# Kernel tuning notes

Measured on AMD Instinct MI355X. Metric: run time of the kernel, lower is better.

## Reference

```python
import jax, jax.numpy as jnp
import numpy as np

B, S, DIM = 2, 2048, 2048
H = 16
Q_LORA, KV_LORA = 1536, 512
D_NOPE, D_ROPE, D_V = 128, 64, 128
D_QK = D_NOPE + D_ROPE  # 192
SCALE = D_QK ** -0.5
EPS = 1e-6
NEG = -1e30


def rmsnorm(x, w):
    return x * jax.lax.rsqrt(jnp.mean(x * x, axis=-1, keepdims=True) + EPS) * w


def apply_rope(x, cos, sin):
    # x: [..., S, ..., d] with adjacent-pair complex layout (torch view_as_complex)
    d2 = x.shape[-1] // 2
    xr = x.reshape(x.shape[:-1] + (d2, 2))
    x0, x1 = xr[..., 0], xr[..., 1]
    bshape = (1, cos.shape[0]) + (1,) * (x.ndim - 3) + (d2,)
    c, s = cos.reshape(bshape), sin.reshape(bshape)
    o0 = x0 * c - x1 * s
    o1 = x0 * s + x1 * c
    return jnp.stack([o0, o1], axis=-1).reshape(x.shape)


def setup_inputs() -> dict:
    key = jax.random.key(0)
    ks = jax.random.split(key, 6)
    inv_freq = 1.0 / (10000.0 ** (np.arange(0, D_ROPE, 2, dtype=np.float32) / D_ROPE))
    ang = np.arange(S, dtype=np.float32)[:, None] * inv_freq[None, :]  # [S, 32]
    return {
        "x": jax.random.normal(ks[0], (B, S, DIM), jnp.float32),
        "wq_a": jax.random.normal(ks[1], (Q_LORA, DIM), jnp.float32) * (DIM ** -0.5),
        "q_norm_w": jnp.ones((Q_LORA,), jnp.float32),
        "wq_b": jax.random.normal(ks[2], (H * D_QK, Q_LORA), jnp.float32) * (Q_LORA ** -0.5),
        "wkv_a": jax.random.normal(ks[3], (KV_LORA + D_ROPE, DIM), jnp.float32) * (DIM ** -0.5),
        "kv_norm_w": jnp.ones((KV_LORA,), jnp.float32),
        "wkv_b": jax.random.normal(ks[4], (H * (D_NOPE + D_V), KV_LORA), jnp.float32) * (KV_LORA ** -0.5),
        "wo": jax.random.normal(ks[5], (DIM, H * D_V), jnp.float32) * ((H * D_V) ** -0.5),
        "cos": jnp.asarray(np.cos(ang)),
        "sin": jnp.asarray(np.sin(ang)),
    }


def reference(x, wq_a, q_norm_w, wq_b, wkv_a, kv_norm_w, wkv_b, wo, cos, sin):
    b, s, _ = x.shape
    # low-rank query projection: wq_b(q_norm(wq_a(x)))
    q = jnp.einsum('bsd,rd->bsr', x, wq_a)
    q = rmsnorm(q, q_norm_w)
    q = jnp.einsum('bsr,or->bso', q, wq_b).reshape(b, s, H, D_QK)
    q_nope, q_pe = q[..., :D_NOPE], q[..., D_NOPE:]
    q_pe = apply_rope(q_pe, cos, sin)  # [b,s,h,64]

    # joint kv latent + rope key
    kv = jnp.einsum('bsd,od->bso', x, wkv_a)
    kv_c, k_pe = kv[..., :KV_LORA], kv[..., KV_LORA:]
    k_pe = apply_rope(k_pe, cos, sin)          # [b,t,64]
    kv_c = rmsnorm(kv_c, kv_norm_w)            # [b,t,c] latent kv cache

    # absorbed wkv_b: [H, d_nope+d_v, c]
    wkv_b_r = wkv_b.reshape(H, D_NOPE + D_V, KV_LORA)
    w_nope, w_v = wkv_b_r[:, :D_NOPE, :], wkv_b_r[:, D_NOPE:, :]

    q_abs = jnp.einsum('bshd,hdc->bshc', q_nope, w_nope)  # absorb K up-proj into q
    scores = (jnp.einsum('bshc,btc->bsht', q_abs, kv_c) +
              jnp.einsum('bshr,btr->bsht', q_pe, k_pe)) * SCALE

    causal = jnp.tril(jnp.ones((s, s), bool))  # [s, t]
    scores = jnp.where(causal[:, None, :], scores, NEG)

    attn = jax.nn.softmax(scores.astype(jnp.float32), axis=-1).astype(x.dtype)
    o = jnp.einsum('bsht,btc->bshc', attn, kv_c)       # attend in latent space
    o = jnp.einsum('bshc,hdc->bshd', o, w_v)           # absorb V up-proj
    out = jnp.einsum('bsf,of->bso', o.reshape(b, s, H * D_V), wo)
    return out
```

## Files before the change

### kernel.cpp

```cpp
#include <hip/hip_runtime.h>
#include <hip/hip_bf16.h>
#include <stdint.h>

#define B_    2
#define S_    2048
#define DIM_  2048
#define H_    16
#define QL_   1536
#define KVL_  512
#define DN_   128
#define DR_   64
#define DV_   128
#define DQK_  192
#define NKV_  576
#define NKVP_ 640
#define BS_   (B_*S_)
#define SCALE_ 0.07216878364870322f

typedef __hip_bfloat16 bf16;
typedef float f32x4 __attribute__((ext_vector_type(4)));
typedef short bf16x8 __attribute__((ext_vector_type(8)));

#define BMT 128
#define BNT 128
#define BKT 64

__device__ __forceinline__ void gload_lds16(const void* g, void* l) {
#if __has_builtin(__builtin_amdgcn_global_load_lds)
  __builtin_amdgcn_global_load_lds(
      (const __attribute__((address_space(1))) void*)g,
      (__attribute__((address_space(3))) void*)l, 16, 0, 0);
#else
  *(uint4*)l = *(const uint4*)g;
#endif
}

template <int K, int LDA, int LDB, int LDC, int FLAGS>
__global__ __launch_bounds__(512, 4) void gemm_t(
    const bf16* __restrict__ A, long saz,
    const bf16* __restrict__ Bm, long sbz,
    void* __restrict__ Cv, long scz,
    void* __restrict__ Cv2)
{
  int z = blockIdx.z;
  A  += (long)z * saz;
  Bm += (long)z * sbz;
  long coff = (long)z * scz;

  int gx = gridDim.x;
  int lin = blockIdx.y * gx + blockIdx.x;
  int nwg = gx * gridDim.y;
  int wg = (lin & 7) * (nwg >> 3) + (lin >> 3);
  int ry = wg / gx, col0 = (wg % gx) * BNT;

  int tid = threadIdx.x, lane = tid & 63, wave = tid >> 6;
  int wm = (wave >> 2) * 64, wn = (wave & 3) * 32;
  int quad = lane >> 4, l16 = lane & 15;

  __shared__ __align__(16) bf16 Asm[BMT * BKT];
  __shared__ __align__(16) bf16 Bsm[BNT * BKT];

  const int npass = (FLAGS & 16) ? 2 : 1;
  const int nty = gridDim.y * ((FLAGS & 16) ? 2 : 1);

  for (int p = 0; p < npass; ++p) {
    int rt = (p == 0) ? ry : (nty - 1 - ry);
    int row0 = rt * BMT;

    if (FLAGS & 2) { if (col0 > row0 + (BMT - 1)) continue; }
    int kend = K;
    if (FLAGS & 4) { int lim = row0 + BMT; if (lim < kend) kend = lim; }

    f32x4 acc[4][2] = {};

    for (int k0 = 0; k0 < kend; k0 += BKT) {
      __syncthreads();
#pragma unroll
      for (int t = 0; t < 2; ++t) {
        int c = (wave * 2 + t) * 64 + lane;
        int m = c >> 3, jx = c & 7, j = jx ^ (m & 7);
        gload_lds16(A  + (long)((row0 + m) * LDA + k0 + j * 8), Asm + c * 8);
        gload_lds16(Bm + (long)((col0 + m) * LDB + k0 + j * 8), Bsm + c * 8);
      }
      __syncthreads();
#pragma unroll
      for (int kk = 0; kk < BKT; kk += 32) {
        int jl = (kk >> 3) + quad;
        bf16x8 af[4], bfv[2];
#pragma unroll
        for (int i = 0; i < 4; ++i) {
          int m = wm + i * 16 + l16;
          af[i]  = *(const bf16x8*)(Asm + m * 64 + ((jl ^ (m & 7)) * 8));
        }
#pragma unroll
        for (int jn = 0; jn < 2; ++jn) {
          int n = wn + jn * 16 + l16;
          bfv[jn] = *(const bf16x8*)(Bsm + n * 64 + ((jl ^ (n & 7)) * 8));
        }
#pragma unroll
        for (int i = 0; i < 4; ++i)
#pragma unroll
          for (int jn = 0; jn < 2; ++jn)
            acc[i][jn] = __builtin_amdgcn_mfma_f32_16x16x32_bf16(af[i], bfv[jn], acc[i][jn], 0, 0, 0);
      }
    }

    if (FLAGS & 128) {
      if (col0 < QL_) {
        bf16* C = (bf16*)Cv;
#pragma unroll
        for (int i = 0; i < 4; ++i)
#pragma unroll
          for (int jn = 0; jn < 2; ++jn)
#pragma unroll
            for (int r = 0; r < 4; ++r) {
              int rr = row0 + wm + i * 16 + quad * 4 + r;
              int cc = col0 + wn + jn * 16 + l16;
              C[(long)rr * QL_ + cc] = __float2bfloat16(acc[i][jn][r]);
            }
      } else {
        float* C2 = (float*)Cv2;
#pragma unroll
        for (int i = 0; i < 4; ++i)
#pragma unroll
          for (int jn = 0; jn < 2; ++jn)
#pragma unroll
            for (int r = 0; r < 4; ++r) {
              int rr = row0 + wm + i * 16 + quad * 4 + r;
              int cc = col0 + wn + jn * 16 + l16 - QL_;
              C2[(long)rr * NKVP_ + cc] = acc[i][jn][r];
            }
      }
    } else if (FLAGS & 256) {
      int cb = col0 >> 7, h = cb >> 1;
      if ((cb & 1) == 0) {
        bf16* C = (bf16*)Cv + ((long)z * H_ + h) * (long)S_ * DQK_;
#pragma unroll
        for (int i = 0; i < 4; ++i)
#pragma unroll
          for (int jn = 0; jn < 2; ++jn)
#pragma unroll
            for (int r = 0; r < 4; ++r) {
              int rr = row0 + wm + i * 16 + quad * 4 + r;
              int cc = (wn + jn * 16 + l16) & 127;
              C[(long)rr * DQK_ + cc] = __float2bfloat16(acc[i][jn][r]);
            }
      } else {
        bf16* C = (bf16*)Cv2 + (long)z * S_ * S_;
#pragma unroll
        for (int i = 0; i < 4; ++i)
#pragma unroll
          for (int jn = 0; jn < 2; ++jn) {
            int rr = row0 + wm + i * 16 + quad * 4;
            int nv = h * 128 + ((wn + jn * 16 + l16) & 127);
            __align__(8) bf16 t4[4];
#pragma unroll
            for (int r = 0; r < 4; ++r) t4[r] = __float2bfloat16(acc[i][jn][r]);
            *(short4*)(C + (long)nv * S_ + rr) = *(const short4*)t4;
          }
      }
    } else if (FLAGS & 1) {
      float* C = (float*)Cv + coff;
#pragma unroll
      for (int i = 0; i < 4; ++i)
#pragma unroll
        for (int jn = 0; jn < 2; ++jn)
#pragma unroll
          for (int r = 0; r < 4; ++r) {
            int rr = row0 + wm + i * 16 + quad * 4 + r;
            int cc = col0 + wn + jn * 16 + l16;
            C[(long)rr * LDC + cc] = acc[i][jn][r];
          }
    } else if (FLAGS & 8) {
      bf16* C = (bf16*)Cv + coff;
#pragma unroll
      for (int i = 0; i < 4; ++i)
#pragma unroll
        for (int jn = 0; jn < 2; ++jn)
#pragma unroll
          for (int r = 0; r < 4; ++r) {
            int rr = row0 + wm + i * 16 + quad * 4 + r;
            int cc = col0 + wn + jn * 16 + l16;
            C[(long)rr * LDC + cc] = __float2bfloat16(acc[i][jn][r] * SCALE_);
          }
    } else {
      bf16* C = (bf16*)Cv + coff;
#pragma unroll
      for (int i = 0; i < 4; ++i)
#pragma unroll
        for (int jn = 0; jn < 2; ++jn)
#pragma unroll
          for (int r = 0; r < 4; ++r) {
            int rr = row0 + wm + i * 16 + quad * 4 + r;
            int cc = col0 + wn + jn * 16 + l16;
            C[(long)rr * LDC + cc] = __float2bfloat16(acc[i][jn][r]);
          }
    }
  }
}

template <int K, int LDA, int LDB, int LDC, int FLAGS>
static inline void G(hipStream_t st, const bf16* A, long saz, const bf16* Bp, long sbz,
                     void* C, long scz, int M, int N, int Z, void* C2 = nullptr) {
  int gy = M / BMT;
  if (FLAGS & 16) gy >>= 1;
  dim3 g(N / BNT, gy, Z);
  gemm_t<K, LDA, LDB, LDC, FLAGS><<<g, 512, 0, st>>>(A, saz, Bp, sbz, C, scz, C2);
}

__device__ __forceinline__ float wsum(float v) {
#pragma unroll
  for (int o = 32; o > 0; o >>= 1) v += __shfl_down(v, o, 64);
  return v;
}

#define CVT_N0  8388608L
#define CVT_N1 11534336L
#define CVT_N2 16252928L
#define CVT_N3 18350080L
#define CVT_N4 22544384L
#define CVT_N5 23855104L
__device__ __forceinline__ void cvt8(const float* __restrict__ s, bf16* __restrict__ d) {
  float4 a = ((const float4*)s)[0], b = ((const float4*)s)[1];
  __align__(16) bf16 t[8];
  t[0] = __float2bfloat16(a.x); t[1] = __float2bfloat16(a.y);
  t[2] = __float2bfloat16(a.z); t[3] = __float2bfloat16(a.w);
  t[4] = __float2bfloat16(b.x); t[5] = __float2bfloat16(b.y);
  t[6] = __float2bfloat16(b.z); t[7] = __float2bfloat16(b.w);
  *(uint4*)d = *(const uint4*)t;
}
__global__ __launch_bounds__(256) void cvt_all(
    const float* __restrict__ x, const float* __restrict__ wq_a,
    const float* __restrict__ wq_b, const float* __restrict__ wkv_b,
    const float* __restrict__ wo, const float* __restrict__ wkv_a,
    bf16* __restrict__ xb, bf16* __restrict__ wqab, bf16* __restrict__ wqbb,
    bf16* __restrict__ wkvbb, bf16* __restrict__ wob, bf16* __restrict__ wkvab)
{
  const long ngrp = CVT_N5 / 8;
  for (long v = (long)blockIdx.x * 256 + threadIdx.x; v < ngrp; v += (long)gridDim.x * 256) {
    long i = v * 8;
    if (i < CVT_N0) {
      cvt8(x + i, xb + i);
    } else if (i < CVT_N1) {
      long j = i - CVT_N0; cvt8(wq_a + j, wqab + j);
    } else if (i < CVT_N2) {
      long j = i - CVT_N1; cvt8(wq_b + j, wqbb + j);
    } else if (i < CVT_N3) {
      long j = i - CVT_N2; cvt8(wkv_b + j, wkvbb + j);
    } else if (i < CVT_N4) {
      long j = i - CVT_N3; cvt8(wo + j, wob + j);
    } else {
      long j = i - CVT_N4;
      if (j < (long)NKV_ * DIM_) cvt8(wkv_a + j, wkvab + j);
      else { __align__(16) bf16 t[8] = {}; *(uint4*)(wkvab + j) = *(const uint4*)t; }
    }
  }
}

__global__ __launch_bounds__(256) void rmsnorm_qa(bf16* __restrict__ qa, const float* __restrict__ w) {
  long row = blockIdx.x;
  bf16* pr = qa + row * QL_;
  int tid = threadIdx.x, lane = tid & 63, wave = tid >> 6;
  float v[6]; float ss = 0.f;
#pragma unroll
  for (int k = 0; k < 6; ++k) { int c = tid + k * 256; v[k] = __bfloat162float(pr[c]); ss += v[k] * v[k]; }
  ss = wsum(ss);
  __shared__ float sred[4];
  if (lane == 0) sred[wave] = ss;
  __syncthreads();
  float tot = sred[0] + sred[1] + sred[2] + sred[3];
  float scl = rsqrtf(tot / (float)QL_ + 1e-6f);
#pragma unroll
  for (int k = 0; k < 6; ++k) { int c = tid + k * 256; pr[c] = __float2bfloat16(v[k] * scl * w[c]); }
}

__global__ __launch_bounds__(256) void kv_post(const float* __restrict__ kvraw, const float* __restrict__ kvw,
                                               const float* __restrict__ cosb, const float* __restrict__ sinb,
                                               bf16* __restrict__ kfull) {
  int bs = blockIdx.x;
  int s = bs & (S_ - 1);
  const float* rowp = kvraw + (long)bs * NKVP_;
  bf16* outp = kfull + (long)bs * NKV_;
  int tid = threadIdx.x, lane = tid & 63, wave = tid >> 6;
  float v0 = rowp[tid], v1 = rowp[tid + 256];
  float ss = v0 * v0 + v1 * v1;
  ss = wsum(ss);
  __shared__ float sred[4];
  if (lane == 0) sred[wave] = ss;
  __syncthreads();
  float tot = sred[0] + sred[1] + sred[2] + sred[3];
  float scl = rsqrtf(tot / (float)KVL_ + 1e-6f);
  outp[tid]       = __float2bfloat16(v0 * scl * kvw[tid]);
  outp[tid + 256] = __float2bfloat16(v1 * scl * kvw[tid + 256]);
  if (tid < 32) {
    float x0 = rowp[KVL_ + 2 * tid], x1 = rowp[KVL_ + 2 * tid + 1];
    float c = cosb[s * 32 + tid], sn = sinb[s * 32 + tid];
    outp[KVL_ + 2 * tid]     = __float2bfloat16(x0 * c - x1 * sn);
    outp[KVL_ + 2 * tid + 1] = __float2bfloat16(x0 * sn + x1 * c);
  }
}

__global__ __launch_bounds__(256) void rope_q(bf16* __restrict__ qb,
                                              const float* __restrict__ cosb,
                                              const float* __restrict__ sinb) {
  int tx = threadIdx.x & 31, ty = threadIdx.x >> 5;
  long row = (long)blockIdx.x * 8 + ty;
  long bs = row >> 4; int h = (int)(row & 15); int s = (int)(bs & (S_ - 1));
  bf16* p = qb + bs * (H_ * DQK_) + h * DQK_ + DN_;
  float x0 = __bfloat162float(p[2 * tx]), x1 = __bfloat162float(p[2 * tx + 1]);
  float c = cosb[s * 32 + tx], sn = sinb[s * 32 + tx];
  p[2 * tx]     = __float2bfloat16(x0 * c - x1 * sn);
  p[2 * tx + 1] = __float2bfloat16(x0 * sn + x1 * c);
}

__global__ __launch_bounds__(256) void kpe_fill(const bf16* __restrict__ kfull, bf16* __restrict__ kvabs) {
  const long n = (long)B_ * H_ * S_ * 64;
  for (long i = (long)blockIdx.x * 256 + threadIdx.x; i < n; i += (long)gridDim.x * 256) {
    int d = (int)(i & 63);
    long t = (i >> 6) & (S_ - 1);
    int h = (int)((i >> 17) & 15);
    int b = (int)(i >> 21);
    kvabs[(((long)(b * H_ + h) * S_) + t) * DQK_ + DN_ + d] =
        kfull[((long)b * S_ + t) * NKV_ + KVL_ + d];
  }
}

__global__ __launch_bounds__(256) void softmax_causal(bf16* __restrict__ sc) {
  int wave = threadIdx.x >> 6, lane = threadIdx.x & 63;
  int r = wave * 512 + blockIdx.x, z = blockIdx.y;
  bf16* row = sc + ((long)z * S_ + r) * S_;
  int wlen = (r & ~127) + 128;
  int base0 = lane * 8;

  float v[4][8];
  float mx = -3.0e38f;
#pragma unroll
  for (int c = 0; c < 4; ++c) {
    int cb = c * 512;
    if (cb <= r) {
      int base = cb + base0;
      __align__(16) bf16 t8[8];
      *(bf16x8*)t8 = *(const bf16x8*)(row + base);
      if (cb + 511 <= r) {
#pragma unroll
        for (int j = 0; j < 8; ++j) {
          float f = __bfloat162float(t8[j]);
          v[c][j] = f; mx = fmaxf(mx, f);
        }
      } else {
#pragma unroll
        for (int j = 0; j < 8; ++j) {
          float f = (base + j <= r) ? __bfloat162float(t8[j]) : -3.0e38f;
          v[c][j] = f; mx = fmaxf(mx, f);
        }
      }
    }
  }
#pragma unroll
  for (int o = 32; o > 0; o >>= 1) mx = fmaxf(mx, __shfl_xor(mx, o, 64));

  float s = 0.f;
#pragma unroll
  for (int c = 0; c < 4; ++c) {
    if (c * 512 <= r) {
#pragma unroll
      for (int j = 0; j < 8; ++j) {
        float e = __expf(v[c][j] - mx);
        v[c][j] = e; s += e;
      }
    }
  }
#pragma unroll
  for (int o = 32; o > 0; o >>= 1) s += __shfl_xor(s, o, 64);
  float inv = 1.f / s;

#pragma unroll
  for (int c = 0; c < 4; ++c) {
    int base = c * 512 + base0;
    if (c * 512 <= r && base < wlen) {
      __align__(16) bf16 t8[8];
#pragma unroll
      for (int j = 0; j < 8; ++j) t8[j] = __float2bfloat16(v[c][j] * inv);
      *(bf16x8*)(row + base) = *(const bf16x8*)t8;
    }
  }
}

template <int HC>
static void attn_loop(hipStream_t stream, const bf16* qb, const bf16* kvabs,
                      const bf16* VabsT,
                      bf16* ovb, bf16* scores_c) {
  const int nch = B_ * (H_ / HC);
  for (int ch = 0; ch < nch; ++ch) {
    int b = ch / (H_ / HC), hq = ch % (H_ / HC), h0 = hq * HC;

    G<DQK_, H_ * DQK_, DQK_, S_, 8 | 2>(stream,
        qb + (long)b * S_ * (H_ * DQK_) + (long)h0 * DQK_, DQK_,
        kvabs + (long)(b * H_ + h0) * S_ * DQK_, (long)S_ * DQK_,
        scores_c, (long)S_ * S_, S_, S_, HC);
    softmax_causal<<<dim3(S_ / 4, HC), 256, 0, stream>>>(scores_c);
    G<S_, S_, S_, H_ * DV_, 4 | 16>(stream,
        scores_c, (long)S_ * S_,
        VabsT + (long)b * S_ * S_ + (long)h0 * DV_ * S_, (long)DV_ * S_,
        ovb + (long)b * S_ * (H_ * DV_) + (long)h0 * DV_, DV_, S_, DV_, HC);
  }
}

extern "C" void kernel_launch(void* const* d_in, const int* in_sizes, int n_in,
                              void* d_out, int out_size, void* d_ws, size_t ws_size,
                              hipStream_t stream) {
  const float* x     = (const float*)d_in[0];
  const float* wq_a  = (const float*)d_in[1];
  const float* qnw   = (const float*)d_in[2];
  const float* wq_b  = (const float*)d_in[3];
  const float* wkv_a = (const float*)d_in[4];
  const float* kvnw  = (const float*)d_in[5];
  const float* wkv_b = (const float*)d_in[6];
  const float* wo    = (const float*)d_in[7];
  const float* cosb  = (const float*)d_in[8];
  const float* sinb  = (const float*)d_in[9];
  float* out = (float*)d_out;
  (void)in_sizes; (void)n_in; (void)out_size;

  int hc;
  if      (ws_size >= 235405312UL) hc = 16;
  else if (ws_size >= 168296448UL) hc = 8;
  else                             hc = 4;

  char* base = (char*)d_ws;
  long off = 0;
  auto at = [&](long bytes) { char* r = base + off; off += bytes; return r; };

  bf16* qb    = (bf16*)at(25165824L);
  bf16* ovb   = (bf16*)at(16777216L);
  bf16* kfull = (bf16*)at(4718592L);
  bf16* wkvbb = (bf16*)at(4194304L);
  bf16* wob   = (bf16*)at(8388608L);
  bf16* kvabs = (bf16*)at(25165824L);
  bf16* VabsT = (bf16*)at(16777216L);
  char* ov = base + off;

  bf16*  xb    = (bf16*) (ov);
  bf16*  wqab  = (bf16*) (ov + 16777216L);
  bf16*  wkvab = (bf16*) (ov + 23068672L);
  bf16*  wqbb  = (bf16*) (ov + 25690112L);
  bf16*  qa    = (bf16*) (ov + 35127296L);
  float* kvraw = (float*)(ov + 47710208L);

  bf16* scores_c = (bf16*)ov;

  cvt_all<<<4096, 256, 0, stream>>>(x, wq_a, wq_b, wkv_b, wo, wkv_a,
                                    xb, wqab, wqbb, wkvbb, wob, wkvab);

  G<DIM_, DIM_, DIM_, QL_, 128>(stream, xb, 0, wqab, 0,
                                qa, 0, BS_, QL_ + NKVP_, 1, kvraw);
  rmsnorm_qa<<<BS_, 256, 0, stream>>>(qa, qnw);
  kv_post<<<BS_, 256, 0, stream>>>(kvraw, kvnw, cosb, sinb, kfull);

  G<QL_, QL_, QL_, H_ * DQK_, 0>(stream, qa, 0, wqbb, 0, qb, 0, BS_, H_ * DQK_, 1);
  rope_q<<<BS_ * H_ / 8, 256, 0, stream>>>(qb, cosb, sinb);

  G<KVL_, NKV_, KVL_, DQK_, 256>(stream,
      kfull, (long)S_ * NKV_, wkvbb, 0,
      kvabs, 0, S_, H_ * 256, B_, VabsT);
  kpe_fill<<<8192, 256, 0, stream>>>(kfull, kvabs);

  if (hc == 16)
    attn_loop<16>(stream, qb, kvabs, VabsT, ovb, scores_c);
  else if (hc == 8)
    attn_loop<8>(stream, qb, kvabs, VabsT, ovb, scores_c);
  else
    attn_loop<4>(stream, qb, kvabs, VabsT, ovb, scores_c);

  G<H_ * DV_, H_ * DV_, H_ * DV_, DIM_, 1>(stream, ovb, 0, wob, 0, out, 0, BS_, DIM_, 1);
}
```

Baseline: 517.8 us.

## Add dedicated causal PV GEMM kernel with 64-row tiles and paired load balancing

Replaces the generic GEMM used for the probability-times-V step with a specialized kernel that uses 64x128 output tiles and stops the K loop at the causal diagonal. Each workgroup handles a mirrored pair of row tiles (rt and 31-rt) so the triangular work is balanced, and workgroup IDs are remapped across 8 groups for locality. The smaller tiles give more parallelism and skip masked-zero work, at the cost of less data reuse per tile and a new hand-written kernel with fixed shape assumptions.

After: 513.8 us. About the same (-0.8%).

```diff
diff --git a/kernel.cpp b/kernel.cpp
--- a/kernel.cpp
+++ b/kernel.cpp
@@ -206,6 +206,83 @@
   if (FLAGS & 16) gy >>= 1;
   dim3 g(N / BNT, gy, Z);
   gemm_t<K, LDA, LDB, LDC, FLAGS><<<g, 512, 0, st>>>(A, saz, Bp, sbz, C, scz, C2);
+}
+
+__global__ __launch_bounds__(512, 4) void pv64_t(
+    const bf16* __restrict__ P,
+    const bf16* __restrict__ Vt,
+    bf16* __restrict__ C)
+{
+  int gx = gridDim.x;
+  int lin = blockIdx.y * gx + blockIdx.x;
+  int nwg = gx * gridDim.y;
+  int wg = (lin & 7) * (nwg >> 3) + (lin >> 3);
+  int ry = wg / gx;
+  int col0 = (wg % gx) * 128;
+  const bf16* A0 = P + (long)(col0 >> 7) * S_ * S_;
+
+  int tid = threadIdx.x, lane = tid & 63, wave = tid >> 6;
+  int wm = (wave >> 2) * 32, wn = (wave & 3) * 32;
+  int quad = lane >> 4, l16 = lane & 15;
+
+  __shared__ __align__(16) bf16 Asm[64 * 64];
+  __shared__ __align__(16) bf16 Bsm[128 * 64];
+
+  for (int p = 0; p < 2; ++p) {
+    int rt = (p == 0) ? ry : (31 - ry);
+    int row0 = rt * 64;
+    int kend = row0 + 64;
+
+    f32x4 acc[2][2] = {};
+
+    for (int k0 = 0; k0 < kend; k0 += 64) {
+      __syncthreads();
+#pragma unroll
+      for (int t = 0; t < 3; ++t) {
+        int c = tid + t * 512;
+        if (c < 512) {
+          int m = c >> 3, j = (c & 7) ^ (m & 7);
+          gload_lds16(A0 + (long)(row0 + m) * S_ + k0 + j * 8, Asm + c * 8);
+        } else {
+          int cb = c - 512;
+          int m = cb >> 3, j = (cb & 7) ^ (m & 7);
+          gload_lds16(Vt + (long)(col0 + m) * S_ + k0 + j * 8, Bsm + cb * 8);
+        }
+      }
+      __syncthreads();
+#pragma unroll
+      for (int kk = 0; kk < 64; kk += 32) {
+        int jl = (kk >> 3) + quad;
+        bf16x8 af[2], bfv[2];
+#pragma unroll
+        for (int i = 0; i < 2; ++i) {
+          int m = wm + i * 16 + l16;
+          af[i] = *(const bf16x8*)(Asm + m * 64 + ((jl ^ (m & 7)) * 8));
+        }
+#pragma unroll
+        for (int jn = 0; jn < 2; ++jn) {
+          int n = wn + jn * 16 + l16;
+          bfv[jn] = *(const bf16x8*)(Bsm + n * 64 + ((jl ^ (n & 7)) * 8));
+        }
+#pragma unroll
+        for (int i = 0; i < 2; ++i)
+#pragma unroll
+          for (int jn = 0; jn < 2; ++jn)
+            acc[i][jn] = __builtin_amdgcn_mfma_f32_16x16x32_bf16(af[i], bfv[jn], acc[i][jn], 0, 0, 0);
+      }
+    }
+
+#pragma unroll
+    for (int i = 0; i < 2; ++i)
+#pragma unroll
+      for (int jn = 0; jn < 2; ++jn)
+#pragma unroll
+        for (int r = 0; r < 4; ++r) {
+          int rr = row0 + wm + i * 16 + quad * 4 + r;
+          int cc = col0 + wn + jn * 16 + l16;
+          C[(long)rr * (H_ * DV_) + cc] = __float2bfloat16(acc[i][jn][r]);
+        }
+  }
 }
 
 __device__ __forceinline__ float wsum(float v) {
@@ -399,10 +476,10 @@
         kvabs + (long)(b * H_ + h0) * S_ * DQK_, (long)S_ * DQK_,
         scores_c, (long)S_ * S_, S_, S_, HC);
     softmax_causal<<<dim3(S_ / 4, HC), 256, 0, stream>>>(scores_c);
-    G<S_, S_, S_, H_ * DV_, 4 | 16>(stream,
-        scores_c, (long)S_ * S_,
-        VabsT + (long)b * S_ * S_ + (long)h0 * DV_ * S_, (long)DV_ * S_,
-        ovb + (long)b * S_ * (H_ * DV_) + (long)h0 * DV_, DV_, S_, DV_, HC);
+    pv64_t<<<dim3(HC, 16, 1), 512, 0, stream>>>(
+        scores_c,
+        VabsT + (long)b * S_ * S_ + (long)h0 * DV_ * S_,
+        ovb + (long)b * S_ * (H_ * DV_) + (long)h0 * DV_);
   }
 }
 
```
